# Kernel tuning notes

Measured on AMD Instinct MI355X. Metric: run time of the kernel, lower is better.

The kernel has to match this reference:

```python
import jax, jax.numpy as jnp
import numpy as np

WEIGHT = 1.0  # configer affinity_loss weight


def setup_inputs() -> dict:
    key = jax.random.key(0)
    k1, k2, k3, k4, k5 = jax.random.split(key, 5)
    bz, C, h, w = 4, 21, 32, 32
    token_n = h * w            # 1024
    total_n = token_n + 1      # 1025 (CLS token in encoder attns)
    head_n = 8
    return {
        "preds": jax.random.normal(k1, (bz, C, h, w), dtype=jnp.float32),
        "low_feats": jnp.zeros((1,), dtype=jnp.float32),
        "high_feats": jnp.zeros((1,), dtype=jnp.float32),
        "unlabeled_ROIs": jax.random.randint(k2, (bz, h, w), 0, 2, dtype=jnp.int32),
        "targets": jax.random.randint(k3, (bz, h, w), 0, C),
        # raw (pre-renormalization) positive attention maps, stacked over 2 layers
        "attns": jax.random.uniform(k4, (2, bz, head_n, total_n, total_n), dtype=jnp.float32),
        "decode_attns": jax.random.uniform(k5, (2, bz, head_n, token_n, token_n), dtype=jnp.float32),
    }


def reference(preds, low_feats, high_feats, unlabeled_ROIs, targets, attns, decode_attns):
    # loss_index=2, gt_add=0
    bz, C, h, w = preds.shape
    token_n = h * w
    Le = attns.shape[0]
    Ld = decode_attns.shape[0]

    # Encoder attentions: drop CLS row/col, row-normalize, average over heads & layers.
    enc = attns[:, :, :, 1:, 1:]                         # (Le, b, H, t, t)
    enc = enc / enc.sum(axis=-1, keepdims=True)
    encode_attn_avg = enc.mean(axis=(0, 2))              # (b, t, t)

    # Decoder attentions: crop to token_n, row-normalize, average over heads & layers.
    dec = decode_attns[:, :, :, :token_n, :token_n]
    dec = dec / dec.sum(axis=-1, keepdims=True)
    decode_attn_avg = dec.mean(axis=(0, 2))              # (b, t, t)

    total_attn_avg = (encode_attn_avg * Le + decode_attn_avg * Ld) / (Le + Ld)

    # Class probabilities per token: (b, t, C)
    prob = jax.nn.softmax(preds, axis=1).reshape(bz, C, token_n).transpose(0, 2, 1)

    # The broadcast-multiply-sum over dim=2 is exactly a batched matmul.
    affinity_prob = jnp.einsum('bij,bjc->bic', total_attn_avg, prob)
    affinity_prob = affinity_prob / affinity_prob.sum(axis=-1, keepdims=True)

    # nearest-interp to (h, w) is the identity here (ROIs already at (h, w))
    roi = unlabeled_ROIs.astype(jnp.float32).reshape(bz, token_n, 1)
    N = roi.sum()
    loss = (roi * jnp.abs(prob - affinity_prob)).sum()
    loss = jnp.where(N > 0, loss / N, loss)
    return WEIGHT * loss
```

## Files before the change

### kernel.cpp

```cpp
#include <hip/hip_runtime.h>
#include <cstdint>
#include <cstddef>

#define C_N     21
#define BZ      4
#define TOKEN_N 1024
#define TOTAL_N 1025
#define PROB_ELEMS (BZ * TOKEN_N * C_N)

typedef short  short8 __attribute__((ext_vector_type(8)));
typedef float  f32x4  __attribute__((ext_vector_type(4)));

static __device__ __forceinline__ unsigned short f2bf(float x) {
    unsigned int u = __float_as_uint(x);
    unsigned int r = (u + 0x7FFFu + ((u >> 16) & 1u)) >> 16;
    return (unsigned short)r;
}

struct __attribute__((packed, aligned(4))) f4u { float x, y, z, w; };

__global__ __launch_bounds__(256) void softmax_kernel(const float* __restrict__ preds,
                                                      float* __restrict__ prob) {
    int t = blockIdx.x * blockDim.x + threadIdx.x;
    if (t >= BZ * TOKEN_N) return;
    int b = t >> 10, j = t & 1023;
    const float* p = preds + (size_t)b * C_N * TOKEN_N + j;
    float v[C_N];
    float mx = -3.4e38f;
#pragma unroll
    for (int c = 0; c < C_N; ++c) { v[c] = p[(size_t)c * TOKEN_N]; mx = fmaxf(mx, v[c]); }
    float ss = 0.f;
#pragma unroll
    for (int c = 0; c < C_N; ++c) { v[c] = __expf(v[c] - mx); ss += v[c]; }
    float inv = 1.f / ss;
    float* o = prob + (size_t)t * C_N;
#pragma unroll
    for (int c = 0; c < C_N; ++c) o[c] = v[c] * inv;
}

__global__ __launch_bounds__(256) void bpack2_kernel(const float* __restrict__ prob,
                                                     uint4* __restrict__ bp) {
    int idx = blockIdx.x * 256 + threadIdx.x;
    if (idx >= BZ * 32 * 2 * 64) return;
    int lane = idx & 63;
    int nt   = (idx >> 6) & 1;
    int kk   = (idx >> 7) & 31;
    int b    = idx >> 12;
    int n    = (lane & 15) + nt * 16;
    int k0   = kk * 32 + ((lane >> 4) << 3);
    unsigned short h[8];
#pragma unroll
    for (int e = 0; e < 8; ++e) {
        float v;
        if (n < C_N)       v = prob[((size_t)b * TOKEN_N + (k0 + e)) * C_N + n];
        else if (n == C_N) v = 1.0f;
        else               v = 0.0f;
        h[e] = f2bf(v);
    }
    uint4 o;
    o.x = h[0] | ((unsigned)h[1] << 16);
    o.y = h[2] | ((unsigned)h[3] << 16);
    o.z = h[4] | ((unsigned)h[5] << 16);
    o.w = h[6] | ((unsigned)h[7] << 16);
    bp[idx] = o;
}

template<bool ENC>
__device__ __forceinline__ void rows_body(const float* __restrict__ base, int mm, int lane,
                                          int i0, const uint4* __restrict__ bp,
                                          float* __restrict__ acc) {
    const int b   = (mm >> 3) & 3;
    const int row = i0 + (lane & 15);
    const int kg8 = (lane >> 4) << 3;
    const float* rowp;
    if constexpr (ENC)
        rowp = base + (size_t)mm * ((size_t)TOTAL_N * TOTAL_N) + (size_t)(row + 1) * TOTAL_N + 1 + kg8;
    else
        rowp = base + (size_t)mm * ((size_t)TOKEN_N * TOKEN_N) + (size_t)row * TOKEN_N + kg8;
    const uint4* bpp = bp + (size_t)b * 4096 + lane;

    f32x4 c0 = {0.f, 0.f, 0.f, 0.f};
    f32x4 c1 = {0.f, 0.f, 0.f, 0.f};

    float a00, a01, a02, a03, a04, a05, a06, a07;
    float a10, a11, a12, a13, a14, a15, a16, a17;
    uint4 B00, B01, B10, B11;

#define LOADA(s, kk) do { const float* p_ = rowp + (kk) * 32;                         \
    if constexpr (ENC) {                                                              \
        f4u u_ = *reinterpret_cast<const f4u*>(p_);                                   \
        f4u v_ = *reinterpret_cast<const f4u*>(p_ + 4);                               \
        a##s##0 = u_.x; a##s##1 = u_.y; a##s##2 = u_.z; a##s##3 = u_.w;               \
        a##s##4 = v_.x; a##s##5 = v_.y; a##s##6 = v_.z; a##s##7 = v_.w;               \
    } else {                                                                          \
        float4 u_ = *reinterpret_cast<const float4*>(p_);                             \
        float4 v_ = *reinterpret_cast<const float4*>(p_ + 4);                         \
        a##s##0 = u_.x; a##s##1 = u_.y; a##s##2 = u_.z; a##s##3 = u_.w;               \
        a##s##4 = v_.x; a##s##5 = v_.y; a##s##6 = v_.z; a##s##7 = v_.w;               \
    } } while (0)

#define COMPUTE(s, BB0, BB1) do {                                                     \
    unsigned w0_ = (unsigned)f2bf(a##s##0) | ((unsigned)f2bf(a##s##1) << 16);         \
    unsigned w1_ = (unsigned)f2bf(a##s##2) | ((unsigned)f2bf(a##s##3) << 16);         \
    unsigned w2_ = (unsigned)f2bf(a##s##4) | ((unsigned)f2bf(a##s##5) << 16);         \
    unsigned w3_ = (unsigned)f2bf(a##s##6) | ((unsigned)f2bf(a##s##7) << 16);         \
    uint4 aw_; aw_.x = w0_; aw_.y = w1_; aw_.z = w2_; aw_.w = w3_;                    \
    short8 af_ = __builtin_bit_cast(short8, aw_);                                     \
    c0 = __builtin_amdgcn_mfma_f32_16x16x32_bf16(af_, __builtin_bit_cast(short8, BB0), c0, 0, 0, 0); \
    c1 = __builtin_amdgcn_mfma_f32_16x16x32_bf16(af_, __builtin_bit_cast(short8, BB1), c1, 0, 0, 0); \
    } while (0)

    LOADA(0, 0); B00 = bpp[0];   B01 = bpp[64];
    LOADA(1, 1); B10 = bpp[128]; B11 = bpp[192];
    for (int kk = 0; kk < 30; kk += 2) {
        COMPUTE(0, B00, B01);
        LOADA(0, kk + 2); B00 = bpp[(kk + 2) * 128]; B01 = bpp[(kk + 2) * 128 + 64];
        COMPUTE(1, B10, B11);
        LOADA(1, kk + 3); B10 = bpp[(kk + 3) * 128]; B11 = bpp[(kk + 3) * 128 + 64];
    }
    COMPUTE(0, B00, B01);
    COMPUTE(1, B10, B11);
#undef LOADA
#undef COMPUTE

    const int grp = lane >> 4, coln = lane & 15;
#pragma unroll
    for (int r = 0; r < 4; ++r) {
        float sv  = __shfl(c1[r], (lane & 48) + 5);
        float inv = 1.0f / sv;
        int i = i0 + grp * 4 + r;
        float* ao = acc + ((size_t)b * TOKEN_N + i) * C_N;
        unsafeAtomicAdd(&ao[coln], c0[r] * inv);
        if (coln < C_N - 16) unsafeAtomicAdd(&ao[16 + coln], c1[r] * inv);
    }
}

__global__ __launch_bounds__(256) void rows4_kernel(const float* __restrict__ attns,
                                                    const float* __restrict__ dattns,
                                                    const uint4* __restrict__ bp,
                                                    float* __restrict__ acc) {
    const int lane = threadIdx.x & 63;
    const int wid  = blockIdx.x * 4 + (threadIdx.x >> 6);
    const int m    = wid >> 6;
    const int i0   = (wid & 63) << 4;
    if (m < 64) rows_body<true >(attns,  m,      lane, i0, bp, acc);
    else        rows_body<false>(dattns, m - 64, lane, i0, bp, acc);
}

__global__ __launch_bounds__(256) void loss_kernel(const float* __restrict__ prob,
                                                   const float* __restrict__ acc,
                                                   const int* __restrict__ roi,
                                                   float* __restrict__ scal) {
    int t = blockIdx.x * 256 + threadIdx.x;
    float lossp = 0.f, np = 0.f;
    if (t < BZ * TOKEN_N) {
        int rv = roi[t];
        np = (float)rv;
        const float* a = acc + (size_t)t * C_N;
        const float* p = prob + (size_t)t * C_N;
        float S = 0.f;
#pragma unroll
        for (int c = 0; c < C_N; ++c) S += a[c];
        float invS = 1.f / S;
        float l = 0.f;
#pragma unroll
        for (int c = 0; c < C_N; ++c) l += fabsf(p[c] - a[c] * invS);
        lossp = rv ? l : 0.f;
    }
#pragma unroll
    for (int off = 32; off > 0; off >>= 1) {
        lossp += __shfl_down(lossp, off);
        np    += __shfl_down(np, off);
    }
    __shared__ float redL[4], redN[4];
    int lane = threadIdx.x & 63, wv = threadIdx.x >> 6;
    if (lane == 0) { redL[wv] = lossp; redN[wv] = np; }
    __syncthreads();
    if (threadIdx.x == 0) {
        float L  = redL[0] + redL[1] + redL[2] + redL[3];
        float NN = redN[0] + redN[1] + redN[2] + redN[3];
        unsafeAtomicAdd(&scal[0], L);
        unsafeAtomicAdd(&scal[1], NN);
    }
}

__global__ void finalize_kernel(const float* __restrict__ scal, float* __restrict__ out) {
    float loss = scal[0], N = scal[1];
    out[0] = (N > 0.f) ? (loss / N) : loss;
}

extern "C" void kernel_launch(void* const* d_in, const int* in_sizes, int n_in,
                              void* d_out, int out_size, void* d_ws, size_t ws_size,
                              hipStream_t stream) {
    const float* preds  = (const float*)d_in[0];
    const int*   roi    = (const int*)d_in[3];
    const float* attns  = (const float*)d_in[5];
    const float* dattns = (const float*)d_in[6];

    float* prob = (float*)d_ws;
    float* acc  = prob + PROB_ELEMS;
    float* scal = acc + PROB_ELEMS;
    uint4* bpack = (uint4*)((char*)d_ws + ((PROB_ELEMS * 2 + 2) * sizeof(float) + 15 & ~(size_t)15));

    hipMemsetAsync(acc, 0, (PROB_ELEMS + 2) * sizeof(float), stream);

    hipLaunchKernelGGL(softmax_kernel, dim3((BZ * TOKEN_N + 255) / 256), dim3(256), 0, stream,
                       preds, prob);
    hipLaunchKernelGGL(bpack2_kernel, dim3(64), dim3(256), 0, stream,
                       prob, bpack);
    hipLaunchKernelGGL(rows4_kernel, dim3(2048), dim3(256), 0, stream,
                       attns, dattns, bpack, acc);
    hipLaunchKernelGGL(loss_kernel, dim3((BZ * TOKEN_N + 255) / 256), dim3(256), 0, stream,
                       prob, acc, roi, scal);
    hipLaunchKernelGGL(finalize_kernel, dim3(1), dim3(1), 0, stream,
                       scal, (float*)d_out);
}
```

Measured before the change: 141.3 us.

## Stage attention tiles through double-buffered LDS with coalesced aligned float4 loads

```diff
diff --git a/kernel.cpp b/kernel.cpp
--- a/kernel.cpp
+++ b/kernel.cpp
@@ -7,17 +7,15 @@
 #define TOKEN_N 1024
 #define TOTAL_N 1025
 #define PROB_ELEMS (BZ * TOKEN_N * C_N)
+#define ENC_TOT  (2u * 4u * 8u * 1050625u)
 
 typedef short  short8 __attribute__((ext_vector_type(8)));
 typedef float  f32x4  __attribute__((ext_vector_type(4)));
 
-static __device__ __forceinline__ unsigned short f2bf(float x) {
+static __device__ __forceinline__ unsigned int f2bf(float x) {
     unsigned int u = __float_as_uint(x);
-    unsigned int r = (u + 0x7FFFu + ((u >> 16) & 1u)) >> 16;
-    return (unsigned short)r;
-}
-
-struct __attribute__((packed, aligned(4))) f4u { float x, y, z, w; };
+    return (u + 0x7FFFu + ((u >> 16) & 1u)) >> 16;
+}
 
 __global__ __launch_bounds__(256) void softmax_kernel(const float* __restrict__ preds,
                                                       float* __restrict__ prob) {
@@ -48,7 +46,7 @@
     int b    = idx >> 12;
     int n    = (lane & 15) + nt * 16;
     int k0   = kk * 32 + ((lane >> 4) << 3);
-    unsigned short h[8];
+    unsigned int h[8];
 #pragma unroll
     for (int e = 0; e < 8; ++e) {
         float v;
@@ -58,93 +56,143 @@
         h[e] = f2bf(v);
     }
     uint4 o;
-    o.x = h[0] | ((unsigned)h[1] << 16);
-    o.y = h[2] | ((unsigned)h[3] << 16);
-    o.z = h[4] | ((unsigned)h[5] << 16);
-    o.w = h[6] | ((unsigned)h[7] << 16);
+    o.x = h[0] | (h[1] << 16);
+    o.y = h[2] | (h[3] << 16);
+    o.z = h[4] | (h[5] << 16);
+    o.w = h[6] | (h[7] << 16);
     bp[idx] = o;
 }
 
 template<bool ENC>
 __device__ __forceinline__ void rows_body(const float* __restrict__ base, int mm, int lane,
                                           int i0, const uint4* __restrict__ bp,
-                                          float* __restrict__ acc) {
-    const int b   = (mm >> 3) & 3;
-    const int row = i0 + (lane & 15);
-    const int kg8 = (lane >> 4) << 3;
-    const float* rowp;
-    if constexpr (ENC)
-        rowp = base + (size_t)mm * ((size_t)TOTAL_N * TOTAL_N) + (size_t)(row + 1) * TOTAL_N + 1 + kg8;
-    else
-        rowp = base + (size_t)mm * ((size_t)TOKEN_N * TOKEN_N) + (size_t)row * TOKEN_N + kg8;
+                                          float* __restrict__ acc, float* __restrict__ ldsw) {
+    constexpr int UPR   = ENC ? 17 : 16;
+    constexpr int RS    = ENC ? 68 : 64;
+    constexpr int NSLOT = ENC ? 5 : 4;
+    const int b = (mm >> 3) & 3;
+
+    const float* gs[5];
+#pragma unroll
+    for (int s = 0; s < NSLOT; ++s) {
+        int t = (ENC && s == 4) ? (256 + (lane & 15)) : (s * 64 + lane);
+        int row = t / UPR;
+        int u   = t - row * UPR;
+        size_t gidx;
+        if constexpr (ENC) {
+            size_t start = (size_t)mm * 1050625u + (size_t)(1 + i0 + row) * 1025u + 1u;
+            int delta = (int)(start & 3);
+            gidx = start - delta + (size_t)u * 4;
+            if (s == 4 && gidx > (size_t)(ENC_TOT - 4)) gidx = ENC_TOT - 4;
+        } else {
+            gidx = (size_t)mm * 1048576u + (size_t)(i0 + row) * 1024u + (size_t)u * 4;
+        }
+        gs[s] = base + gidx;
+    }
+
+    float4 G[5];
+    auto LOADG = [&](int ch) {
+#pragma unroll
+        for (int s = 0; s < NSLOT; ++s)
+            G[s] = *reinterpret_cast<const float4*>(gs[s] + ch * 64);
+    };
+    auto WRITEG = [&](int buf) {
+        float* d = ldsw + buf * 1088;
+#pragma unroll
+        for (int s = 0; s < NSLOT; ++s) {
+            int t = (ENC && s == 4) ? (256 + (lane & 15)) : (s * 64 + lane);
+            *reinterpret_cast<float4*>(d + (size_t)t * 4) = G[s];
+        }
+    };
+
     const uint4* bpp = bp + (size_t)b * 4096 + lane;
+    uint4 B0, B1, B2, B3, N0, N1, N2, N3;
+    auto LOADBN = [&](int ch) {
+        N0 = bpp[ch * 256];       N1 = bpp[ch * 256 + 64];
+        N2 = bpp[ch * 256 + 128]; N3 = bpp[ch * 256 + 192];
+    };
+
+    const int r = lane & 15, kg = lane >> 4;
+    int fragbase;
+    if constexpr (ENC) fragbase = r * RS + ((mm + i0 + r + 2) & 3) + kg * 8;
+    else               fragbase = r * RS + kg * 8;
 
     f32x4 c0 = {0.f, 0.f, 0.f, 0.f};
     f32x4 c1 = {0.f, 0.f, 0.f, 0.f};
-
-    float a00, a01, a02, a03, a04, a05, a06, a07;
-    float a10, a11, a12, a13, a14, a15, a16, a17;
-    uint4 B00, B01, B10, B11;
-
-#define LOADA(s, kk) do { const float* p_ = rowp + (kk) * 32;                         \
-    if constexpr (ENC) {                                                              \
-        f4u u_ = *reinterpret_cast<const f4u*>(p_);                                   \
-        f4u v_ = *reinterpret_cast<const f4u*>(p_ + 4);                               \
-        a##s##0 = u_.x; a##s##1 = u_.y; a##s##2 = u_.z; a##s##3 = u_.w;               \
-        a##s##4 = v_.x; a##s##5 = v_.y; a##s##6 = v_.z; a##s##7 = v_.w;               \
-    } else {                                                                          \
-        float4 u_ = *reinterpret_cast<const float4*>(p_);                             \
-        float4 v_ = *reinterpret_cast<const float4*>(p_ + 4);                         \
-        a##s##0 = u_.x; a##s##1 = u_.y; a##s##2 = u_.z; a##s##3 = u_.w;               \
-        a##s##4 = v_.x; a##s##5 = v_.y; a##s##6 = v_.z; a##s##7 = v_.w;               \
-    } } while (0)
-
-#define COMPUTE(s, BB0, BB1) do {                                                     \
-    unsigned w0_ = (unsigned)f2bf(a##s##0) | ((unsigned)f2bf(a##s##1) << 16);         \
-    unsigned w1_ = (unsigned)f2bf(a##s##2) | ((unsigned)f2bf(a##s##3) << 16);         \
-    unsigned w2_ = (unsigned)f2bf(a##s##4) | ((unsigned)f2bf(a##s##5) << 16);         \
-    unsigned w3_ = (unsigned)f2bf(a##s##6) | ((unsigned)f2bf(a##s##7) << 16);         \
-    uint4 aw_; aw_.x = w0_; aw_.y = w1_; aw_.z = w2_; aw_.w = w3_;                    \
-    short8 af_ = __builtin_bit_cast(short8, aw_);                                     \
-    c0 = __builtin_amdgcn_mfma_f32_16x16x32_bf16(af_, __builtin_bit_cast(short8, BB0), c0, 0, 0, 0); \
-    c1 = __builtin_amdgcn_mfma_f32_16x16x32_bf16(af_, __builtin_bit_cast(short8, BB1), c1, 0, 0, 0); \
-    } while (0)
-
-    LOADA(0, 0); B00 = bpp[0];   B01 = bpp[64];
-    LOADA(1, 1); B10 = bpp[128]; B11 = bpp[192];
-    for (int kk = 0; kk < 30; kk += 2) {
-        COMPUTE(0, B00, B01);
-        LOADA(0, kk + 2); B00 = bpp[(kk + 2) * 128]; B01 = bpp[(kk + 2) * 128 + 64];
-        COMPUTE(1, B10, B11);
-        LOADA(1, kk + 3); B10 = bpp[(kk + 3) * 128]; B11 = bpp[(kk + 3) * 128 + 64];
-    }
-    COMPUTE(0, B00, B01);
-    COMPUTE(1, B10, B11);
-#undef LOADA
-#undef COMPUTE
-
-    const int grp = lane >> 4, coln = lane & 15;
-#pragma unroll
-    for (int r = 0; r < 4; ++r) {
-        float sv  = __shfl(c1[r], (lane & 48) + 5);
+    auto KSTEP = [&](const float* lf, int j0, uint4 bb0, uint4 bb1) {
+        float a0, a1, a2, a3, a4, a5, a6, a7;
+        if constexpr (ENC) {
+            const float* p = lf + fragbase + j0;
+            a0 = p[0]; a1 = p[1]; a2 = p[2]; a3 = p[3];
+            a4 = p[4]; a5 = p[5]; a6 = p[6]; a7 = p[7];
+        } else {
+            float4 lo = *reinterpret_cast<const float4*>(lf + fragbase + j0);
+            float4 hi = *reinterpret_cast<const float4*>(lf + fragbase + j0 + 4);
+            a0 = lo.x; a1 = lo.y; a2 = lo.z; a3 = lo.w;
+            a4 = hi.x; a5 = hi.y; a6 = hi.z; a7 = hi.w;
+        }
+        uint4 aw;
+        aw.x = f2bf(a0) | (f2bf(a1) << 16);
+        aw.y = f2bf(a2) | (f2bf(a3) << 16);
+        aw.z = f2bf(a4) | (f2bf(a5) << 16);
+        aw.w = f2bf(a6) | (f2bf(a7) << 16);
+        short8 af = __builtin_bit_cast(short8, aw);
+        c0 = __builtin_amdgcn_mfma_f32_16x16x32_bf16(af, __builtin_bit_cast(short8, bb0), c0, 0, 0, 0);
+        c1 = __builtin_amdgcn_mfma_f32_16x16x32_bf16(af, __builtin_bit_cast(short8, bb1), c1, 0, 0, 0);
+    };
+
+    LOADG(0); LOADBN(0);
+    B0 = N0; B1 = N1; B2 = N2; B3 = N3;
+    WRITEG(0);
+    LOADG(1); LOADBN(1);
+
+#pragma unroll 2
+    for (int ch = 0; ch < 14; ++ch) {
+        const int cur = ch & 1;
+        const float* lf = ldsw + cur * 1088;
+        KSTEP(lf, 0,  B0, B1);
+        KSTEP(lf, 32, B2, B3);
+        WRITEG(cur ^ 1);
+        B0 = N0; B1 = N1; B2 = N2; B3 = N3;
+        LOADG(ch + 2); LOADBN(ch + 2);
+    }
+    {
+        const float* lf = ldsw + 0 * 1088;
+        KSTEP(lf, 0,  B0, B1);
+        KSTEP(lf, 32, B2, B3);
+        WRITEG(1);
+        B0 = N0; B1 = N1; B2 = N2; B3 = N3;
+    }
+    {
+        const float* lf = ldsw + 1 * 1088;
+        KSTEP(lf, 0,  B0, B1);
+        KSTEP(lf, 32, B2, B3);
+    }
+
+#pragma unroll
+    for (int rr = 0; rr < 4; ++rr) {
+        float sv  = __shfl(c1[rr], (lane & 48) + 5);
         float inv = 1.0f / sv;
-        int i = i0 + grp * 4 + r;
+        int i = i0 + kg * 4 + rr;
         float* ao = acc + ((size_t)b * TOKEN_N + i) * C_N;
-        unsafeAtomicAdd(&ao[coln], c0[r] * inv);
-        if (coln < C_N - 16) unsafeAtomicAdd(&ao[16 + coln], c1[r] * inv);
-    }
-}
-
-__global__ __launch_bounds__(256) void rows4_kernel(const float* __restrict__ attns,
+        unsafeAtomicAdd(&ao[r], c0[rr] * inv);
+        if (r < C_N - 16) unsafeAtomicAdd(&ao[16 + r], c1[rr] * inv);
+    }
+}
+
+__global__ __launch_bounds__(256) void rows5_kernel(const float* __restrict__ attns,
                                                     const float* __restrict__ dattns,
                                                     const uint4* __restrict__ bp,
                                                     float* __restrict__ acc) {
+    __shared__ __align__(16) float lds[8704];
     const int lane = threadIdx.x & 63;
-    const int wid  = blockIdx.x * 4 + (threadIdx.x >> 6);
+    const int wv   = threadIdx.x >> 6;
+    float* ldsw = lds + wv * 2176;
+    const int wid  = blockIdx.x * 4 + wv;
     const int m    = wid >> 6;
     const int i0   = (wid & 63) << 4;
-    if (m < 64) rows_body<true >(attns,  m,      lane, i0, bp, acc);
-    else        rows_body<false>(dattns, m - 64, lane, i0, bp, acc);
+    if (m < 64) rows_body<true >(attns,  m,      lane, i0, bp, acc, ldsw);
+    else        rows_body<false>(dattns, m - 64, lane, i0, bp, acc, ldsw);
 }
 
 __global__ __launch_bounds__(256) void loss_kernel(const float* __restrict__ prob,
@@ -208,7 +256,7 @@
                        preds, prob);
     hipLaunchKernelGGL(bpack2_kernel, dim3(64), dim3(256), 0, stream,
                        prob, bpack);
-    hipLaunchKernelGGL(rows4_kernel, dim3(2048), dim3(256), 0, stream,
+    hipLaunchKernelGGL(rows5_kernel, dim3(2048), dim3(256), 0, stream,
                        attns, dattns, bpack, acc);
     hipLaunchKernelGGL(loss_kernel, dim3((BZ * TOKEN_N + 255) / 256), dim3(256), 0, stream,
                        prob, acc, roi, scal);
```

Result: faster. 129.9 us (-8.1%).
